# Kernel tuning notes

Measured on AMD Instinct MI355X. Metric: run time of the kernel, lower is better.

## Reference

```python
import jax, jax.numpy as jnp
import numpy as np

EPS = 1e-5


def _edge_conv(x, W, gamma, beta, k):
    """x: (B,N,C); W: (O,2C). Returns (B,N,O)."""
    xx = jnp.sum(x * x, axis=2, keepdims=True)                 # (B,N,1)
    inner = jnp.einsum('bnc,bmc->bnm', x, x)                   # (B,N,N)
    dist = xx + jnp.swapaxes(xx, 1, 2) - 2.0 * inner           # squared dists
    idx = jax.lax.top_k(-dist, k)[1]                           # (B,N,k) smallest dists
    nbr = jax.vmap(lambda xb, ib: xb[ib])(x, idx)              # (B,N,k,C) gather
    xi = jnp.broadcast_to(x[:, :, None, :], nbr.shape)
    edge = jnp.concatenate([nbr - xi, xi], axis=-1)            # (B,N,k,2C)
    out = jnp.einsum('bnkc,oc->bnko', edge, W)                 # 1x1 conv (per-edge linear)
    mean = jnp.mean(out, axis=(0, 1, 2))                       # BatchNorm2d (training stats)
    var = jnp.var(out, axis=(0, 1, 2))
    out = (out - mean) / jnp.sqrt(var + EPS) * gamma + beta
    return jnp.max(jax.nn.relu(out), axis=2)                   # max over k -> (B,N,O)


def _layernorm(x, g, b):
    mu = jnp.mean(x, axis=-1, keepdims=True)
    v = jnp.var(x, axis=-1, keepdims=True)
    return (x - mu) / jnp.sqrt(v + EPS) * g + b


def setup_inputs() -> dict:
    key = jax.random.key(0)
    ks = jax.random.split(key, 12)
    B, N = 8, 2048
    C1, C2, C3, C4 = 64, 64, 128, 256
    feat = C1 + C2 + C3 + C4              # 512
    fc_in = 2 * feat                      # max+avg -> 1024
    H, L = 512, 256

    def w(k_, shape):
        fan_in = shape[-1]
        return jax.random.normal(k_, shape, dtype=jnp.float32) * (1.0 / np.sqrt(fan_in))

    return {
        'points': jax.random.normal(ks[0], (B, N, 3), dtype=jnp.float32),
        'W1': w(ks[1], (C1, 6)),  'g1': jnp.ones(C1), 'b1': jnp.zeros(C1),
        'W2': w(ks[2], (C2, 2 * C1)), 'g2': jnp.ones(C2), 'b2': jnp.zeros(C2),
        'W3': w(ks[3], (C3, 2 * C2)), 'g3': jnp.ones(C3), 'b3': jnp.zeros(C3),
        'W4': w(ks[4], (C4, 2 * C3)), 'g4': jnp.ones(C4), 'b4': jnp.zeros(C4),
        'fc1_w': w(ks[5], (H, fc_in)), 'fc1_b': jnp.zeros(H),
        'ln1_g': jnp.ones(H), 'ln1_b': jnp.zeros(H),
        'fc2_w': w(ks[6], (L, H)), 'fc2_b': jnp.zeros(L),
        'ln2_g': jnp.ones(L), 'ln2_b': jnp.zeros(L),
        'k': 20,
    }


def reference(points, W1, g1, b1, W2, g2, b2, W3, g3, b3, W4, g4, b4,
              fc1_w, fc1_b, ln1_g, ln1_b, fc2_w, fc2_b, ln2_g, ln2_b, k):
    x1 = _edge_conv(points, W1, g1, b1, k)   # (B,N,64)
    x2 = _edge_conv(x1, W2, g2, b2, k)       # (B,N,64)
    x3 = _edge_conv(x2, W3, g3, b3, k)       # (B,N,128)
    x4 = _edge_conv(x3, W4, g4, b4, k)       # (B,N,256)
    feat = jnp.concatenate([x1, x2, x3, x4], axis=-1)          # (B,N,512)
    g = jnp.concatenate([jnp.max(feat, axis=1), jnp.mean(feat, axis=1)], axis=-1)  # (B,1024)
    h = g @ fc1_w.T + fc1_b
    h = jax.nn.relu(_layernorm(h, ln1_g, ln1_b))
    z = h @ fc2_w.T + fc2_b
    return _layernorm(z, ln2_g, ln2_b)       # (B,256)
```

## Files before the change

kernel.cpp:

```cpp
#include <hip/hip_runtime.h>
#include <cstdint>
#include <cstddef>

static constexpr int Bb = 8;
static constexpr int Nn = 2048;
static constexpr int Kn = 20;
static constexpr float EPSV = 1e-5f;


struct TransJobs {
    const float* in[6];
    float* out[6];
    int R[6];
    int Cc[6];
};

__global__ void transpose_all_kernel(TransJobs tj) {
    int m = blockIdx.y;
    int i = blockIdx.x * 256 + threadIdx.x;
    int total = tj.R[m] * tj.Cc[m];
    if (i < total) {
        int r = i / tj.Cc[m], c = i % tj.Cc[m];
        tj.out[m][(size_t)c * tj.R[m] + r] = tj.in[m][i];
    }
}


template<int C, int O>
__global__ void prep_kernel(const float* __restrict__ x, const float* __restrict__ wt,
                            float* __restrict__ z1, float* __restrict__ z2,
                            float* __restrict__ xx, float4* __restrict__ xp,
                            float* __restrict__ zp) {
    const int blk = blockIdx.x;
    const int tid = threadIdx.x;
    if (blk >= 1088) {
        zp[(blk - 1088) * 256 + tid] = 0.f;
        return;
    }
    if (blk >= 1024) {
        int i = (blk - 1024) * 256 + tid;
        const float* xr = x + (size_t)i * C;
        float s = 0.f;
        for (int c = 0; c < C; ++c) { float v = xr[c]; s += v * v; }
        xx[i] = s;
        if (C == 3) xp[i] = make_float4(xr[0], xr[1], xr[2], s);
        return;
    }
    constexpr int TP = 16;
    constexpr int G = 256 / O;
    constexpr int PP = TP / G;
    const int p0 = blk * TP;
    const int oo = tid % O;
    const int g = tid / O;
    __shared__ float xs[TP][(C < 4) ? 4 : C];
    for (int e = tid; e < TP * C; e += 256) {
        int p = e / C, c = e % C;
        xs[p][c] = x[(size_t)(p0 + p) * C + c];
    }
    __syncthreads();
    float a1[PP], a2[PP];
#pragma unroll
    for (int p = 0; p < PP; ++p) { a1[p] = 0.f; a2[p] = 0.f; }
    if constexpr (C % 4 == 0) {
        for (int c = 0; c < C; c += 4) {
            float w1[4], w2[4];
#pragma unroll
            for (int q = 0; q < 4; ++q) {
                w1[q] = wt[(size_t)(c + q) * O + oo];
                w2[q] = wt[(size_t)(C + c + q) * O + oo];
            }
#pragma unroll
            for (int p = 0; p < PP; ++p) {
                const float4 xv = *(const float4*)(&xs[g * PP + p][c]);
                a1[p] = fmaf(xv.w, w1[3], fmaf(xv.z, w1[2], fmaf(xv.y, w1[1], fmaf(xv.x, w1[0], a1[p]))));
                a2[p] = fmaf(xv.w, w2[3], fmaf(xv.z, w2[2], fmaf(xv.y, w2[1], fmaf(xv.x, w2[0], a2[p]))));
            }
        }
    } else {
        for (int c = 0; c < C; ++c) {
            float w1 = wt[(size_t)c * O + oo];
            float w2 = wt[(size_t)(C + c) * O + oo];
#pragma unroll
            for (int p = 0; p < PP; ++p) {
                float xv = xs[g * PP + p][c];
                a1[p] = fmaf(xv, w1, a1[p]);
                a2[p] = fmaf(xv, w2, a2[p]);
            }
        }
    }
#pragma unroll
    for (int p = 0; p < PP; ++p) {
        size_t row = (size_t)(p0 + g * PP + p) * O + oo;
        z1[row] = a1[p];
        z2[row] = a2[p];
    }
}


using half8 = __attribute__((ext_vector_type(8))) _Float16;
using f32x16 = __attribute__((ext_vector_type(16))) float;

template<int C>
__global__ __launch_bounds__(256, 2)
void gram_dist_kernel(const float* __restrict__ x, const float* __restrict__ xx,
                      float* __restrict__ dist, int b0, size_t dstride) {
    static_assert(C % 32 == 0, "CT=32 tiling");
    constexpr int CT = 32;
    const int b = b0 + blockIdx.z;
    int p = blockIdx.x, rblk = 0;
    while (p >= 16 - rblk) { p -= 16 - rblk; ++rblk; }
    const int cblk = rblk + p;
    const int i0 = rblk * 128, j0 = cblk * 128;
    const int tid = threadIdx.x;
    const int lane = tid & 63;
    const int wv = tid >> 6;
    const int wr = wv >> 1, wc = wv & 1;

    __shared__ __align__(16) unsigned char smem[32768];
    _Float16* const AH = (_Float16*)smem;
    _Float16* const AL = AH + 4096;
    _Float16* const BH = AH + 8192;
    _Float16* const BL = AH + 12288;
    float (*T)[132] = (float (*)[132])smem;

    const float* xb = x + (size_t)b * Nn * C;
    int sga[4];
    const float* sgs[4];
#pragma unroll
    for (int q = 0; q < 4; ++q) {
        int g = tid + 256 * q;
        int pnt = (g >> 2) & 127;
        int cb8 = g & 3;
        sga[q] = cb8 * 128 + (pnt & ~7) + ((pnt + 2 * cb8) & 7);
        sgs[q] = xb + (size_t)(((q < 2) ? i0 : j0) + pnt) * C + cb8 * 8;
    }

    int fa[2][2], fb[2][2];
#pragma unroll
    for (int ks = 0; ks < 2; ++ks)
#pragma unroll
        for (int mi = 0; mi < 2; ++mi) {
            int t8 = ks * 2 + (lane >> 5);
            int pa = wr * 64 + mi * 32 + (lane & 31);
            int pb = wc * 64 + mi * 32 + (lane & 31);
            fa[ks][mi] = t8 * 128 + (pa & ~7) + ((pa + 2 * t8) & 7);
            fb[ks][mi] = t8 * 128 + (pb & ~7) + ((pb + 2 * t8) & 7);
        }

    f32x16 ahh[2][2] = {};
    f32x16 axx[2][2] = {};

    for (int c0 = 0; c0 < C; c0 += CT) {
#pragma unroll
        for (int q = 0; q < 4; ++q) {
            const float4 f0 = *(const float4*)(sgs[q] + c0);
            const float4 f1 = *(const float4*)(sgs[q] + c0 + 4);
            float v[8] = {f0.x, f0.y, f0.z, f0.w, f1.x, f1.y, f1.z, f1.w};
            half8 hv, lv;
#pragma unroll
            for (int e = 0; e < 8; ++e) {
                _Float16 h = (_Float16)v[e];
                hv[e] = h;
                lv[e] = (_Float16)((v[e] - (float)h) * 4096.f);
            }
            _Float16* dh = (q < 2) ? AH : BH;
            _Float16* dl = (q < 2) ? AL : BL;
            *(half8*)(dh + sga[q] * 8) = hv;
            *(half8*)(dl + sga[q] * 8) = lv;
        }
        __syncthreads();
#pragma unroll
        for (int ks = 0; ks < 2; ++ks) {
            half8 ah[2], al[2], bh[2], bl[2];
#pragma unroll
            for (int mi = 0; mi < 2; ++mi) {
                ah[mi] = *(const half8*)(AH + fa[ks][mi] * 8);
                al[mi] = *(const half8*)(AL + fa[ks][mi] * 8);
                bh[mi] = *(const half8*)(BH + fb[ks][mi] * 8);
                bl[mi] = *(const half8*)(BL + fb[ks][mi] * 8);
            }
#pragma unroll
            for (int mi = 0; mi < 2; ++mi)
#pragma unroll
                for (int ni = 0; ni < 2; ++ni) {
                    ahh[mi][ni] = __builtin_amdgcn_mfma_f32_32x32x16_f16(ah[mi], bh[ni], ahh[mi][ni], 0, 0, 0);
                    axx[mi][ni] = __builtin_amdgcn_mfma_f32_32x32x16_f16(ah[mi], bl[ni], axx[mi][ni], 0, 0, 0);
                    axx[mi][ni] = __builtin_amdgcn_mfma_f32_32x32x16_f16(al[mi], bh[ni], axx[mi][ni], 0, 0, 0);
                }
        }
        __syncthreads();
    }

    const float* xxb = xx + (size_t)b * Nn;
    float xi[2][16];
#pragma unroll
    for (int mi = 0; mi < 2; ++mi)
#pragma unroll
        for (int g = 0; g < 4; ++g) {
            float4 t4 = *(const float4*)(xxb + i0 + wr * 64 + mi * 32 + 4 * (lane >> 5) + 8 * g);
            xi[mi][g * 4 + 0] = t4.x; xi[mi][g * 4 + 1] = t4.y;
            xi[mi][g * 4 + 2] = t4.z; xi[mi][g * 4 + 3] = t4.w;
        }
    float xj[2];
#pragma unroll
    for (int ni = 0; ni < 2; ++ni) xj[ni] = xxb[j0 + wc * 64 + ni * 32 + (lane & 31)];

    float* db = dist + (size_t)blockIdx.z * dstride;
#pragma unroll
    for (int mi = 0; mi < 2; ++mi)
#pragma unroll
        for (int ni = 0; ni < 2; ++ni) {
            const int col = j0 + wc * 64 + ni * 32 + (lane & 31);
#pragma unroll
            for (int r = 0; r < 16; ++r) {
                int row = i0 + wr * 64 + mi * 32 + (r & 3) + 8 * (r >> 2) + 4 * (lane >> 5);
                float inner = fmaf(axx[mi][ni][r], 2.44140625e-4f, ahh[mi][ni][r]);
                db[(size_t)row * Nn + col] = xi[mi][r] + xj[ni] - 2.f * inner;
            }
        }

    if (cblk > rblk) {
        const int rr = tid >> 3;
        const int c4 = (tid & 7) * 4;
#pragma unroll
        for (int m = 0; m < 4; ++m) {
            if (wc == (m >> 1)) {
#pragma unroll
                for (int mi = 0; mi < 2; ++mi)
#pragma unroll
                    for (int r = 0; r < 16; ++r) {
                        int ig = wr * 64 + mi * 32 + (r & 3) + 8 * (r >> 2) + 4 * (lane >> 5);
                        if ((m & 1) == 0) {
                            float inner = fmaf(axx[mi][0][r], 2.44140625e-4f, ahh[mi][0][r]);
                            T[lane & 31][ig] = xi[mi][r] + xj[0] - 2.f * inner;
                        } else {
                            float inner = fmaf(axx[mi][1][r], 2.44140625e-4f, ahh[mi][1][r]);
                            T[lane & 31][ig] = xi[mi][r] + xj[1] - 2.f * inner;
                        }
                    }
            }
            __syncthreads();
            float* orow = db + (size_t)(j0 + m * 32 + rr) * Nn + i0;
#pragma unroll
            for (int s = 0; s < 4; ++s)
                *(float4*)(orow + c4 + s * 32) = *(const float4*)&T[rr][c4 + s * 32];
            __syncthreads();
        }
    }
}


template<int CTRL>
__device__ __forceinline__ float dpp_min_step(float v) {
    int x = __float_as_int(v);
    int y = __builtin_amdgcn_update_dpp(x, x, CTRL, 0xf, 0xf, false);
    return fminf(v, __int_as_float(y));
}

__device__ __forceinline__ float wave_min64(float v) {
    v = dpp_min_step<0x111>(v);
    v = dpp_min_step<0x112>(v);
    v = dpp_min_step<0x114>(v);
    v = dpp_min_step<0x118>(v);
    v = dpp_min_step<0x142>(v);
    v = dpp_min_step<0x143>(v);
    return __int_as_float(__builtin_amdgcn_readlane(__float_as_int(v), 63));
}

__device__ __forceinline__ float pack_key(float v, int m) {
    return __int_as_float((__float_as_int(v) & ~31) | m);
}

#define TOP4_INS(v)                                                               \
    {                                                                             \
        bool l3 = (v) < tv3;                                                      \
        if (l3) {                                                                 \
            bool l2 = (v) < tv2;                                                  \
            bool l1 = (v) < tv1;                                                  \
            bool l0 = (v) < tv0;                                                  \
            tv3 = l2 ? tv2 : (v);                                                 \
            tv2 = l2 ? (l1 ? tv1 : (v)) : tv2;                                    \
            tv1 = l1 ? (l0 ? tv0 : (v)) : tv1;                                    \
            tv0 = l0 ? (v) : tv0;                                                 \
        }                                                                         \
    }

__device__ __forceinline__ void top4_build(const float4* __restrict__ dr4, int lane,
                                           float lvk,
                                           float& tv0, float& tv1, float& tv2, float& tv3) {
    tv0 = tv1 = tv2 = tv3 = 3e38f;
#pragma unroll
    for (int q = 0; q < 8; ++q) {
        float4 f = dr4[q * 64 + lane];
        float vv[4] = {f.x, f.y, f.z, f.w};
#pragma unroll
        for (int c = 0; c < 4; ++c) {
            float vk = pack_key(vv[c], q * 4 + c);
            if (vk > lvk) TOP4_INS(vk)
        }
    }
}

#define TOPK_ROUNDS(REBUILD, DECODE)                                              \
    int myj = 0;                                                                  \
    for (int t = 0; t < Kn; ++t) {                                                \
        float bv = wave_min64(tv0);                                               \
        unsigned long long tied = __ballot(tv0 == bv);                            \
        int wl = (int)(__ffsll((long long)tied) - 1);                             \
        int bm = __float_as_int(bv) & 31;                                         \
        int bj = (DECODE);                                                        \
        if (lane == t) myj = bj;                                                  \
        if (tv0 == bv && lane == wl) {                                            \
            tv0 = tv1; tv1 = tv2; tv2 = tv3; tv3 = 3e38f;                         \
            if (tv0 == 3e38f) { REBUILD; }                                        \
        }                                                                         \
    }                                                                             \
    if (lane < Kn) orow[lane] = myj;

__global__ void topk_kernel(const float* __restrict__ dist, int* __restrict__ idxo,
                            int b0, size_t dstride, int rows_per_batch_only) {
    const int w = threadIdx.x >> 6;
    const int lane = threadIdx.x & 63;
    const int lin = blockIdx.x * 4 + w;
    int bz, i;
    if (rows_per_batch_only) { bz = 0; i = lin; }
    else { bz = lin >> 11; i = lin & (Nn - 1); }
    const int b = b0 + bz;
    const float4* dr4 = (const float4*)(dist + (size_t)bz * dstride + (size_t)i * Nn);

    float tv0, tv1, tv2, tv3;
    top4_build(dr4, lane, -3e38f, tv0, tv1, tv2, tv3);

    int* orow = idxo + ((size_t)b * Nn + i) * Kn;
    TOPK_ROUNDS(top4_build(dr4, lane, bv, tv0, tv1, tv2, tv3),
                (bm >> 2) * 256 + wl * 4 + (bm & 3))
}


__device__ __forceinline__ void top4_build_c3(const float4* __restrict__ xpb,
                                              float xi0, float xi1, float xi2, float xxi,
                                              int lane, float lvk,
                                              float& tv0, float& tv1, float& tv2, float& tv3) {
    tv0 = tv1 = tv2 = tv3 = 3e38f;
#pragma unroll
    for (int m = 0; m < 32; ++m) {
        float4 f = xpb[m * 64 + lane];
        float acc = 0.f;
        acc = fmaf(xi0, f.x, acc);
        acc = fmaf(xi1, f.y, acc);
        acc = fmaf(xi2, f.z, acc);
        float v = xxi + f.w - 2.f * acc;
        float vk = pack_key(v, m);
        if (vk > lvk) TOP4_INS(vk)
    }
}

__global__ void topk_c3_kernel(const float4* __restrict__ xp, int* __restrict__ idxo,
                               int b0, int rows_per_batch_only) {
    const int w = threadIdx.x >> 6;
    const int lane = threadIdx.x & 63;
    const int lin = blockIdx.x * 4 + w;
    int bz, i;
    if (rows_per_batch_only) { bz = 0; i = lin; }
    else { bz = lin >> 11; i = lin & (Nn - 1); }
    const int b = b0 + bz;
    const float4* xpb = xp + (size_t)b * Nn;
    const float4 fi = xpb[i];
    const float xi0 = fi.x, xi1 = fi.y, xi2 = fi.z, xxi = fi.w;

    float tv0, tv1, tv2, tv3;
    top4_build_c3(xpb, xi0, xi1, xi2, xxi, lane, -3e38f, tv0, tv1, tv2, tv3);

    int* orow = idxo + ((size_t)b * Nn + i) * Kn;
    TOPK_ROUNDS(top4_build_c3(xpb, xi0, xi1, xi2, xxi, lane, bv, tv0, tv1, tv2, tv3),
                bm * 64 + wl)
}


template<int O>
__global__ void edge_stats_kernel(const float* __restrict__ z1, const float* __restrict__ z2,
                                  const int* __restrict__ idx,
                                  float* __restrict__ vmax, float* __restrict__ vmin,
                                  float* __restrict__ ssum, float* __restrict__ ssq) {
    constexpr int TPP = O / 4;
    constexpr int PPB = 256 / TPP;
    const int p0 = blockIdx.x * PPB;
    const int tid = threadIdx.x;
    const int q = tid % TPP;
    const int p = tid / TPP;
    const int oo = q * 4;
    __shared__ int jl[PPB][Kn];
    for (int e = tid; e < PPB * Kn; e += 256)
        jl[e / Kn][e % Kn] = idx[(size_t)(p0 + e / Kn) * Kn + (e % Kn)];
    __syncthreads();
    const int bi = p0 + p;
    const int b = bi >> 11;
    const float4 zi1 = *(const float4*)(z1 + (size_t)bi * O + oo);
    const float4 zi2 = *(const float4*)(z2 + (size_t)bi * O + oo);
    float ax = zi2.x - zi1.x, ay = zi2.y - zi1.y, az = zi2.z - zi1.z, aw = zi2.w - zi1.w;
    float mxx = -3e38f, mxy = -3e38f, mxz = -3e38f, mxw = -3e38f;
    float mnx = 3e38f, mny = 3e38f, mnz = 3e38f, mnw = 3e38f;
    float sx = 0.f, sy = 0.f, sz = 0.f, sw = 0.f;
    float qx = 0.f, qy = 0.f, qz = 0.f, qw = 0.f;
    const float* zbase = z1 + ((size_t)b * Nn) * O + oo;
#pragma unroll
    for (int kk = 0; kk < Kn; ++kk) {
        int j = jl[p][kk];
        float4 v = *(const float4*)(zbase + (size_t)j * O);
        v.x += ax; v.y += ay; v.z += az; v.w += aw;
        mxx = fmaxf(mxx, v.x); mxy = fmaxf(mxy, v.y); mxz = fmaxf(mxz, v.z); mxw = fmaxf(mxw, v.w);
        mnx = fminf(mnx, v.x); mny = fminf(mny, v.y); mnz = fminf(mnz, v.z); mnw = fminf(mnw, v.w);
        sx += v.x; sy += v.y; sz += v.z; sw += v.w;
        qx = fmaf(v.x, v.x, qx); qy = fmaf(v.y, v.y, qy);
        qz = fmaf(v.z, v.z, qz); qw = fmaf(v.w, v.w, qw);
    }
    float4 mx4 = make_float4(mxx, mxy, mxz, mxw);
    float4 mn4 = make_float4(mnx, mny, mnz, mnw);
    *(float4*)(vmax + (size_t)bi * O + oo) = mx4;
    *(float4*)(vmin + (size_t)bi * O + oo) = mn4;
    __shared__ float4 ssm[256], sqq[256];
    ssm[tid] = make_float4(sx, sy, sz, sw);
    sqq[tid] = make_float4(qx, qy, qz, qw);
    __syncthreads();
    if (p == 0) {
#pragma unroll 4
        for (int pp = 1; pp < PPB; ++pp) {
            float4 s4 = ssm[pp * TPP + q];
            float4 q4 = sqq[pp * TPP + q];
            sx += s4.x; sy += s4.y; sz += s4.z; sw += s4.w;
            qx += q4.x; qy += q4.y; qz += q4.z; qw += q4.w;
        }
        int slot = blockIdx.x & 63;
        atomicAdd(&ssum[slot * O + oo + 0], sx);
        atomicAdd(&ssum[slot * O + oo + 1], sy);
        atomicAdd(&ssum[slot * O + oo + 2], sz);
        atomicAdd(&ssum[slot * O + oo + 3], sw);
        atomicAdd(&ssq[slot * O + oo + 0], qx);
        atomicAdd(&ssq[slot * O + oo + 1], qy);
        atomicAdd(&ssq[slot * O + oo + 2], qz);
        atomicAdd(&ssq[slot * O + oo + 3], qw);
    }
}


template<int O>
__global__ void apply_pool_kernel(const float* __restrict__ vmax, const float* __restrict__ vmin,
                                  const float* __restrict__ ssum, const float* __restrict__ ssq,
                                  const float* __restrict__ gamma, const float* __restrict__ beta,
                                  float* __restrict__ xout,
                                  float* __restrict__ pmax, float* __restrict__ psum, int obase) {
    constexpr int TPP = O / 4;
    constexpr int PP2 = 256 / TPP;
    constexpr int S = 128 / PP2;
    const int chunk = blockIdx.x;
    const int b = blockIdx.y;
    const int tid = threadIdx.x;
    const int q = tid % TPP;
    const int g = tid / TPP;
    const int oo = q * 4;
    __shared__ __align__(16) float lsc[O], lsh[O];
    for (int o = tid; o < O; o += 256) {
        float s = 0.f, qq = 0.f;
        for (int sl = 0; sl < 64; ++sl) { s += ssum[sl * O + o]; qq += ssq[sl * O + o]; }
        const float cnt = (float)Bb * (float)Nn * (float)Kn;
        float mu = s / cnt;
        float var = qq / cnt - mu * mu;
        float sc_ = gamma[o] / sqrtf(var + EPSV);
        lsc[o] = sc_;
        lsh[o] = beta[o] - mu * sc_;
    }
    __syncthreads();
    const float4 sc = *(const float4*)(lsc + oo);
    const float4 sh = *(const float4*)(lsh + oo);
    float pmx = -3e38f, pmy = -3e38f, pmz = -3e38f, pmw = -3e38f;
    float psx = 0.f, psy = 0.f, psz = 0.f, psw = 0.f;
    const int n0 = chunk * 128;
    for (int s = 0; s < S; ++s) {
        int n = n0 + g + s * PP2;
        size_t ix = ((size_t)b * Nn + n) * O + oo;
        float4 vx = *(const float4*)(vmax + ix);
        float4 vn = *(const float4*)(vmin + ix);
        float4 r;
        r.x = fmaxf(fmaf(sc.x >= 0.f ? vx.x : vn.x, sc.x, sh.x), 0.f);
        r.y = fmaxf(fmaf(sc.y >= 0.f ? vx.y : vn.y, sc.y, sh.y), 0.f);
        r.z = fmaxf(fmaf(sc.z >= 0.f ? vx.z : vn.z, sc.z, sh.z), 0.f);
        r.w = fmaxf(fmaf(sc.w >= 0.f ? vx.w : vn.w, sc.w, sh.w), 0.f);
        *(float4*)(xout + ix) = r;
        pmx = fmaxf(pmx, r.x); pmy = fmaxf(pmy, r.y);
        pmz = fmaxf(pmz, r.z); pmw = fmaxf(pmw, r.w);
        psx += r.x; psy += r.y; psz += r.z; psw += r.w;
    }
    __shared__ float4 sm[256], ss2[256];
    sm[tid] = make_float4(pmx, pmy, pmz, pmw);
    ss2[tid] = make_float4(psx, psy, psz, psw);
    __syncthreads();
    if (g == 0) {
#pragma unroll 4
        for (int gg = 1; gg < PP2; ++gg) {
            float4 m4 = sm[gg * TPP + q];
            float4 s4 = ss2[gg * TPP + q];
            pmx = fmaxf(pmx, m4.x); pmy = fmaxf(pmy, m4.y);
            pmz = fmaxf(pmz, m4.z); pmw = fmaxf(pmw, m4.w);
            psx += s4.x; psy += s4.y; psz += s4.z; psw += s4.w;
        }
        size_t pb = ((size_t)b * 16 + chunk) * 512 + obase + oo;
        *(float4*)(pmax + pb) = make_float4(pmx, pmy, pmz, pmw);
        *(float4*)(psum + pb) = make_float4(psx, psy, psz, psw);
    }
}


__global__ void head1_kernel(const float* __restrict__ pmax, const float* __restrict__ psum,
                             const float* __restrict__ fct1, float* __restrict__ hp1) {
    const int ks = blockIdx.x;
    const int b = blockIdx.y;
    const int tid = threadIdx.x;
    __shared__ float gxs[64];
    if (tid < 64) {
        int c = ks * 64 + tid;
        if (c < 512) {
            float mx = -3e38f;
            for (int ch = 0; ch < 16; ++ch)
                mx = fmaxf(mx, pmax[((size_t)b * 16 + ch) * 512 + c]);
            gxs[tid] = mx;
        } else {
            int e = c - 512;
            float s = 0.f;
            for (int ch = 0; ch < 16; ++ch)
                s += psum[((size_t)b * 16 + ch) * 512 + e];
            gxs[tid] = s * (1.f / (float)Nn);
        }
    }
    __syncthreads();
    float h0 = 0.f, h1 = 0.f;
    const float* w = fct1 + (size_t)(ks * 64) * 512;
    for (int c = 0; c < 64; ++c) {
        float gc = gxs[c];
        h0 = fmaf(gc, w[(size_t)c * 512 + tid], h0);
        h1 = fmaf(gc, w[(size_t)c * 512 + tid + 256], h1);
    }
    hp1[((size_t)b * 16 + ks) * 512 + tid] = h0;
    hp1[((size_t)b * 16 + ks) * 512 + tid + 256] = h1;
}

__global__ void head2_kernel(const float* __restrict__ hp1, const float* __restrict__ fc1b,
                             const float* __restrict__ ln1g, const float* __restrict__ ln1b,
                             float* __restrict__ hh) {
    const int b = blockIdx.x;
    const int tid = threadIdx.x;
    __shared__ float red[256];
    float h0 = fc1b[tid], h1 = fc1b[tid + 256];
    for (int ks = 0; ks < 16; ++ks) {
        h0 += hp1[((size_t)b * 16 + ks) * 512 + tid];
        h1 += hp1[((size_t)b * 16 + ks) * 512 + tid + 256];
    }
    red[tid] = h0 + h1;
    __syncthreads();
    for (int st = 128; st > 0; st >>= 1) { if (tid < st) red[tid] += red[tid + st]; __syncthreads(); }
    float mu = red[0] * (1.f / 512.f);
    __syncthreads();
    float d0 = h0 - mu, d1 = h1 - mu;
    red[tid] = d0 * d0 + d1 * d1;
    __syncthreads();
    for (int st = 128; st > 0; st >>= 1) { if (tid < st) red[tid] += red[tid + st]; __syncthreads(); }
    float rs = 1.f / sqrtf(red[0] * (1.f / 512.f) + EPSV);
    hh[(size_t)b * 512 + tid]       = fmaxf(d0 * rs * ln1g[tid] + ln1b[tid], 0.f);
    hh[(size_t)b * 512 + tid + 256] = fmaxf(d1 * rs * ln1g[tid + 256] + ln1b[tid + 256], 0.f);
}

__global__ void head3_kernel(const float* __restrict__ hh, const float* __restrict__ fct2,
                             float* __restrict__ hp2) {
    const int ks = blockIdx.x;
    const int b = blockIdx.y;
    const int tid = threadIdx.x;
    __shared__ float hs[128];
    if (tid < 128) hs[tid] = hh[(size_t)b * 512 + ks * 128 + tid];
    __syncthreads();
    float z = 0.f;
    const float* w = fct2 + (size_t)(ks * 128) * 256;
    for (int c = 0; c < 128; ++c)
        z = fmaf(hs[c], w[(size_t)c * 256 + tid], z);
    hp2[((size_t)b * 4 + ks) * 256 + tid] = z;
}

__global__ void head4_kernel(const float* __restrict__ hp2, const float* __restrict__ fc2b,
                             const float* __restrict__ ln2g, const float* __restrict__ ln2b,
                             float* __restrict__ out) {
    const int b = blockIdx.x;
    const int tid = threadIdx.x;
    __shared__ float red[256];
    float z = fc2b[tid];
    for (int ks = 0; ks < 4; ++ks) z += hp2[((size_t)b * 4 + ks) * 256 + tid];
    red[tid] = z;
    __syncthreads();
    for (int st = 128; st > 0; st >>= 1) { if (tid < st) red[tid] += red[tid + st]; __syncthreads(); }
    float mu2 = red[0] * (1.f / 256.f);
    __syncthreads();
    float dz = z - mu2;
    red[tid] = dz * dz;
    __syncthreads();
    for (int st = 128; st > 0; st >>= 1) { if (tid < st) red[tid] += red[tid + st]; __syncthreads(); }
    float rs2 = 1.f / sqrtf(red[0] * (1.f / 256.f) + EPSV);
    out[b * 256 + tid] = dz * rs2 * ln2g[tid] + ln2b[tid];
}


template<int C, int O>
static void run_layer(const float* x, const float* gamma, const float* beta,
                      float* xout, float* DIST, float* XX, float4* XP, int* IDX,
                      float* Z1, float* Z2,
                      float* VMX, float* VMN, float* SSUM, float* SSQ,
                      const float* WT, float* PMAX, float* PSUM, int obase, bool big,
                      hipStream_t stream) {
    prep_kernel<C, O><<<1216, 256, 0, stream>>>(x, WT, Z1, Z2, XX, XP, SSUM);
    if constexpr (C == 3) {
        if (big) {
            topk_c3_kernel<<<Bb * Nn / 4, 256, 0, stream>>>(XP, IDX, 0, 0);
        } else {
            for (int b = 0; b < Bb; ++b)
                topk_c3_kernel<<<Nn / 4, 256, 0, stream>>>(XP, IDX, b, 1);
        }
    } else {
        if (big) {
            gram_dist_kernel<C><<<dim3(136, 1, Bb), 256, 0, stream>>>(x, XX, DIST, 0, (size_t)Nn * Nn);
            topk_kernel<<<Bb * Nn / 4, 256, 0, stream>>>(DIST, IDX, 0, (size_t)Nn * Nn, 0);
        } else {
            for (int b = 0; b < Bb; ++b) {
                gram_dist_kernel<C><<<dim3(136, 1, 1), 256, 0, stream>>>(x, XX, DIST, b, 0);
                topk_kernel<<<Nn / 4, 256, 0, stream>>>(DIST, IDX, b, 0, 1);
            }
        }
    }
    edge_stats_kernel<O><<<Bb * Nn / (1024 / O), 256, 0, stream>>>(Z1, Z2, IDX, VMX, VMN, SSUM, SSQ);
    apply_pool_kernel<O><<<dim3(16, 8), 256, 0, stream>>>(VMX, VMN, SSUM, SSQ, gamma, beta,
                                                          xout, PMAX, PSUM, obase);
}

extern "C" void kernel_launch(void* const* d_in, const int* in_sizes, int n_in,
                              void* d_out, int out_size, void* d_ws, size_t ws_size,
                              hipStream_t stream) {
    const float* points = (const float*)d_in[0];
    const float* W1 = (const float*)d_in[1];
    const float* g1 = (const float*)d_in[2];
    const float* b1 = (const float*)d_in[3];
    const float* W2 = (const float*)d_in[4];
    const float* g2 = (const float*)d_in[5];
    const float* b2 = (const float*)d_in[6];
    const float* W3 = (const float*)d_in[7];
    const float* g3 = (const float*)d_in[8];
    const float* b3 = (const float*)d_in[9];
    const float* W4 = (const float*)d_in[10];
    const float* g4 = (const float*)d_in[11];
    const float* b4 = (const float*)d_in[12];
    const float* fc1_w = (const float*)d_in[13];
    const float* fc1_b = (const float*)d_in[14];
    const float* ln1g = (const float*)d_in[15];
    const float* ln1b = (const float*)d_in[16];
    const float* fc2_w = (const float*)d_in[17];
    const float* fc2_b = (const float*)d_in[18];
    const float* ln2g = (const float*)d_in[19];
    const float* ln2b = (const float*)d_in[20];

    float* ws = (float*)d_ws;
    const size_t BN = (size_t)Bb * Nn;
    const bool big = ws_size >= (size_t)59826688 * 4;

    size_t off = 0;
    auto take = [&](size_t n) { size_t o = off; off += n; return o; };
    float* DIST = ws + take(big ? (size_t)Bb * Nn * Nn : (size_t)Nn * Nn);
    float* XX   = ws + take(BN);
    float4* XP  = (float4*)(ws + take(BN * 4));
    int*   IDX  = (int*)(ws + take(BN * Kn));
    float* Z1   = ws + take(BN * 256);
    float* Z2   = ws + take(BN * 256);
    float* VMX  = ws + take(BN * 256);
    float* VMN  = ws + take(BN * 256);
    float* SSUM = ws + take(64 * 256);
    float* SSQ  = ws + take(64 * 256);
    float* WT1  = ws + take(384);
    float* WT2  = ws + take(8192);
    float* WT3  = ws + take(16384);
    float* WT4  = ws + take(65536);
    float* FCT1 = ws + take(524288);
    float* FCT2 = ws + take(131072);
    float* X1   = ws + take(BN * 64);
    float* X2   = ws + take(BN * 64);
    float* X3   = ws + take(BN * 128);
    float* X4   = ws + take(BN * 256);
    float* PMAX = ws + take((size_t)Bb * 16 * 512);
    float* PSUM = ws + take((size_t)Bb * 16 * 512);

    float* HP1 = DIST;
    float* HH  = DIST + 65536;
    float* HP2 = DIST + 65536 + 4096;

    TransJobs tj;
    tj.in[0] = W1;    tj.out[0] = WT1;  tj.R[0] = 64;  tj.Cc[0] = 6;
    tj.in[1] = W2;    tj.out[1] = WT2;  tj.R[1] = 64;  tj.Cc[1] = 128;
    tj.in[2] = W3;    tj.out[2] = WT3;  tj.R[2] = 128; tj.Cc[2] = 128;
    tj.in[3] = W4;    tj.out[3] = WT4;  tj.R[3] = 256; tj.Cc[3] = 256;
    tj.in[4] = fc1_w; tj.out[4] = FCT1; tj.R[4] = 512; tj.Cc[4] = 1024;
    tj.in[5] = fc2_w; tj.out[5] = FCT2; tj.R[5] = 256; tj.Cc[5] = 512;
    transpose_all_kernel<<<dim3(2048, 6), 256, 0, stream>>>(tj);

    run_layer<3, 64>(points, g1, b1, X1, DIST, XX, XP, IDX, Z1, Z2, VMX, VMN, SSUM, SSQ, WT1, PMAX, PSUM, 0, big, stream);
    run_layer<64, 64>(X1, g2, b2, X2, DIST, XX, XP, IDX, Z1, Z2, VMX, VMN, SSUM, SSQ, WT2, PMAX, PSUM, 64, big, stream);
    run_layer<64, 128>(X2, g3, b3, X3, DIST, XX, XP, IDX, Z1, Z2, VMX, VMN, SSUM, SSQ, WT3, PMAX, PSUM, 128, big, stream);
    run_layer<128, 256>(X3, g4, b4, X4, DIST, XX, XP, IDX, Z1, Z2, VMX, VMN, SSUM, SSQ, WT4, PMAX, PSUM, 256, big, stream);

    head1_kernel<<<dim3(16, 8), 256, 0, stream>>>(PMAX, PSUM, FCT1, HP1);
    head2_kernel<<<Bb, 256, 0, stream>>>(HP1, fc1_b, ln1g, ln1b, HH);
    head3_kernel<<<dim3(4, 8), 256, 0, stream>>>(HH, FCT2, HP2);
    head4_kernel<<<Bb, 256, 0, stream>>>(HP2, fc2_b, ln2g, ln2b, (float*)d_out);
}
```

Baseline: 542.1 us.

## Compute per-point edge projections with split-fp16 MFMA instead of scalar FMA

For layers 2-4, the per-point projections Z1/Z2 (x times the two halves of W) are now computed with 32x32x16 fp16 MFMA instructions. Each fp32 input is split into a high fp16 part and a scaled low residual, and three MFMA products keep close to fp32 accuracy. A new prep kernel does the split into the DIST scratch buffer and also computes the squared norms and zeroes the stats. This replaces the scalar FMA GEMM and the weight transposes for those layers, at the cost of an extra kernel launch, extra memory traffic for the split buffers, and a small accuracy risk.

```diff
diff --git a/kernel.cpp b/kernel.cpp
--- a/kernel.cpp
+++ b/kernel.cpp
@@ -24,6 +24,9 @@
         tj.out[m][(size_t)c * tj.R[m] + r] = tj.in[m][i];
     }
 }
+
+using half8 = __attribute__((ext_vector_type(8))) _Float16;
+using f32x16 = __attribute__((ext_vector_type(16))) float;
 
 
 template<int C, int O>
@@ -61,31 +64,14 @@
     float a1[PP], a2[PP];
 #pragma unroll
     for (int p = 0; p < PP; ++p) { a1[p] = 0.f; a2[p] = 0.f; }
-    if constexpr (C % 4 == 0) {
-        for (int c = 0; c < C; c += 4) {
-            float w1[4], w2[4];
-#pragma unroll
-            for (int q = 0; q < 4; ++q) {
-                w1[q] = wt[(size_t)(c + q) * O + oo];
-                w2[q] = wt[(size_t)(C + c + q) * O + oo];
-            }
-#pragma unroll
-            for (int p = 0; p < PP; ++p) {
-                const float4 xv = *(const float4*)(&xs[g * PP + p][c]);
-                a1[p] = fmaf(xv.w, w1[3], fmaf(xv.z, w1[2], fmaf(xv.y, w1[1], fmaf(xv.x, w1[0], a1[p]))));
-                a2[p] = fmaf(xv.w, w2[3], fmaf(xv.z, w2[2], fmaf(xv.y, w2[1], fmaf(xv.x, w2[0], a2[p]))));
-            }
-        }
-    } else {
-        for (int c = 0; c < C; ++c) {
-            float w1 = wt[(size_t)c * O + oo];
-            float w2 = wt[(size_t)(C + c) * O + oo];
-#pragma unroll
-            for (int p = 0; p < PP; ++p) {
-                float xv = xs[g * PP + p][c];
-                a1[p] = fmaf(xv, w1, a1[p]);
-                a2[p] = fmaf(xv, w2, a2[p]);
-            }
+    for (int c = 0; c < C; ++c) {
+        float w1 = wt[(size_t)c * O + oo];
+        float w2 = wt[(size_t)(C + c) * O + oo];
+#pragma unroll
+        for (int p = 0; p < PP; ++p) {
+            float xv = xs[g * PP + p][c];
+            a1[p] = fmaf(xv, w1, a1[p]);
+            a2[p] = fmaf(xv, w2, a2[p]);
         }
     }
 #pragma unroll
@@ -97,8 +83,90 @@
 }
 
 
-using half8 = __attribute__((ext_vector_type(8))) _Float16;
-using f32x16 = __attribute__((ext_vector_type(16))) float;
+template<int C, int O>
+__global__ void slim_prep_kernel(const float* __restrict__ x, const float* __restrict__ w,
+                                 _Float16* __restrict__ xh, _Float16* __restrict__ xl,
+                                 _Float16* __restrict__ wh, _Float16* __restrict__ wl,
+                                 float* __restrict__ xx, float* __restrict__ zp) {
+    constexpr int NXS = (Bb * Nn * C) / 2048;
+    constexpr int NWS = (O * 2 * C) / 2048;
+    static_assert((Bb * Nn * C) % 2048 == 0 && (O * 2 * C) % 2048 == 0, "split tiling");
+    const int blk = blockIdx.x;
+    const int tid = threadIdx.x;
+    if (blk < NXS + NWS) {
+        const bool isw = blk >= NXS;
+        const float* src = isw ? w : x;
+        _Float16* dh = isw ? wh : xh;
+        _Float16* dl = isw ? wl : xl;
+        size_t idx = ((size_t)(isw ? blk - NXS : blk) * 256 + tid) * 8;
+        float4 f0 = *(const float4*)(src + idx);
+        float4 f1 = *(const float4*)(src + idx + 4);
+        float v[8] = {f0.x, f0.y, f0.z, f0.w, f1.x, f1.y, f1.z, f1.w};
+        half8 hv, lv;
+#pragma unroll
+        for (int e = 0; e < 8; ++e) {
+            _Float16 h = (_Float16)v[e];
+            hv[e] = h;
+            lv[e] = (_Float16)((v[e] - (float)h) * 4096.f);
+        }
+        *(half8*)(dh + idx) = hv;
+        *(half8*)(dl + idx) = lv;
+        return;
+    }
+    int b2 = blk - NXS - NWS;
+    if (b2 < 64) {
+        int i = b2 * 256 + tid;
+        const float* xr = x + (size_t)i * C;
+        float s = 0.f;
+        for (int c = 0; c < C; ++c) { float v = xr[c]; s += v * v; }
+        xx[i] = s;
+        return;
+    }
+    zp[(b2 - 64) * 256 + tid] = 0.f;
+}
+
+
+template<int C, int O>
+__global__ __launch_bounds__(256)
+void zmfma_kernel(const _Float16* __restrict__ xh, const _Float16* __restrict__ xl,
+                  const _Float16* __restrict__ wh, const _Float16* __restrict__ wl,
+                  float* __restrict__ z1, float* __restrict__ z2) {
+    static_assert(C % 16 == 0 && O % 32 == 0, "tiling");
+    const int tid = threadIdx.x;
+    const int lane = tid & 63;
+    const int wv = tid >> 6;
+    const int wr = wv >> 1, wc = wv & 1;
+    const int p = blockIdx.x * 64 + wr * 32 + (lane & 31);
+    const int gcol = blockIdx.y * 64 + wc * 32 + (lane & 31);
+    const int s = (gcol >= O) ? 1 : 0;
+    const int o = gcol - s * O;
+    const int k8 = (lane >> 5) * 8;
+    const _Float16* ap_h = xh + (size_t)p * C + k8;
+    const _Float16* ap_l = xl + (size_t)p * C + k8;
+    const _Float16* bp_h = wh + (size_t)o * (2 * C) + s * C + k8;
+    const _Float16* bp_l = wl + (size_t)o * (2 * C) + s * C + k8;
+
+    f32x16 hh = {};
+    f32x16 xs = {};
+#pragma unroll
+    for (int k = 0; k < C; k += 16) {
+        half8 ah = *(const half8*)(ap_h + k);
+        half8 al = *(const half8*)(ap_l + k);
+        half8 bh = *(const half8*)(bp_h + k);
+        half8 bl = *(const half8*)(bp_l + k);
+        hh = __builtin_amdgcn_mfma_f32_32x32x16_f16(ah, bh, hh, 0, 0, 0);
+        xs = __builtin_amdgcn_mfma_f32_32x32x16_f16(ah, bl, xs, 0, 0, 0);
+        xs = __builtin_amdgcn_mfma_f32_32x32x16_f16(al, bh, xs, 0, 0, 0);
+    }
+    float* out = s ? z2 : z1;
+    const int rbase = blockIdx.x * 64 + wr * 32 + 4 * (lane >> 5);
+#pragma unroll
+    for (int r = 0; r < 16; ++r) {
+        int row = rbase + (r & 3) + 8 * (r >> 2);
+        out[(size_t)row * O + o] = fmaf(xs[r], 2.44140625e-4f, hh[r]);
+    }
+}
+
 
 template<int C>
 __global__ __launch_bounds__(256, 2)
@@ -606,14 +674,14 @@
 
 
 template<int C, int O>
-static void run_layer(const float* x, const float* gamma, const float* beta,
+static void run_layer(const float* x, const float* W, const float* gamma, const float* beta,
                       float* xout, float* DIST, float* XX, float4* XP, int* IDX,
                       float* Z1, float* Z2,
                       float* VMX, float* VMN, float* SSUM, float* SSQ,
                       const float* WT, float* PMAX, float* PSUM, int obase, bool big,
                       hipStream_t stream) {
-    prep_kernel<C, O><<<1216, 256, 0, stream>>>(x, WT, Z1, Z2, XX, XP, SSUM);
     if constexpr (C == 3) {
+        prep_kernel<C, O><<<1216, 256, 0, stream>>>(x, WT, Z1, Z2, XX, XP, SSUM);
         if (big) {
             topk_c3_kernel<<<Bb * Nn / 4, 256, 0, stream>>>(XP, IDX, 0, 0);
         } else {
@@ -621,6 +689,16 @@
                 topk_c3_kernel<<<Nn / 4, 256, 0, stream>>>(XP, IDX, b, 1);
         }
     } else {
+        _Float16* XH = (_Float16*)DIST;
+        _Float16* XL = XH + (size_t)Bb * Nn * C;
+        _Float16* WH = XL + (size_t)Bb * Nn * C;
+        _Float16* WL = WH + (size_t)O * 2 * C;
+        constexpr int NXS = (Bb * Nn * C) / 2048;
+        constexpr int NWS = (O * 2 * C) / 2048;
+        slim_prep_kernel<C, O><<<NXS + NWS + 64 + 128, 256, 0, stream>>>(
+            x, W, XH, XL, WH, WL, XX, SSUM);
+        zmfma_kernel<C, O><<<dim3(Bb * Nn / 64, 2 * O / 64), 256, 0, stream>>>(
+            XH, XL, WH, WL, Z1, Z2);
         if (big) {
             gram_dist_kernel<C><<<dim3(136, 1, Bb), 256, 0, stream>>>(x, XX, DIST, 0, (size_t)Nn * Nn);
             topk_kernel<<<Bb * Nn / 4, 256, 0, stream>>>(DIST, IDX, 0, (size_t)Nn * Nn, 0);
@@ -689,6 +767,7 @@
     float* X4   = ws + take(BN * 256);
     float* PMAX = ws + take((size_t)Bb * 16 * 512);
     float* PSUM = ws + take((size_t)Bb * 16 * 512);
+    (void)WT2; (void)WT3; (void)WT4;
 
     float* HP1 = DIST;
     float* HH  = DIST + 65536;
@@ -696,17 +775,14 @@
 
     TransJobs tj;
     tj.in[0] = W1;    tj.out[0] = WT1;  tj.R[0] = 64;  tj.Cc[0] = 6;
-    tj.in[1] = W2;    tj.out[1] = WT2;  tj.R[1] = 64;  tj.Cc[1] = 128;
-    tj.in[2] = W3;    tj.out[2] = WT3;  tj.R[2] = 128; tj.Cc[2] = 128;
-    tj.in[3] = W4;    tj.out[3] = WT4;  tj.R[3] = 256; tj.Cc[3] = 256;
-    tj.in[4] = fc1_w; tj.out[4] = FCT1; tj.R[4] = 512; tj.Cc[4] = 1024;
-    tj.in[5] = fc2_w; tj.out[5] = FCT2; tj.R[5] = 256; tj.Cc[5] = 512;
-    transpose_all_kernel<<<dim3(2048, 6), 256, 0, stream>>>(tj);
-
-    run_layer<3, 64>(points, g1, b1, X1, DIST, XX, XP, IDX, Z1, Z2, VMX, VMN, SSUM, SSQ, WT1, PMAX, PSUM, 0, big, stream);
-    run_layer<64, 64>(X1, g2, b2, X2, DIST, XX, XP, IDX, Z1, Z2, VMX, VMN, SSUM, SSQ, WT2, PMAX, PSUM, 64, big, stream);
-    run_layer<64, 128>(X2, g3, b3, X3, DIST, XX, XP, IDX, Z1, Z2, VMX, VMN, SSUM, SSQ, WT3, PMAX, PSUM, 128, big, stream);
-    run_layer<128, 256>(X3, g4, b4, X4, DIST, XX, XP, IDX, Z1, Z2, VMX, VMN, SSUM, SSQ, WT4, PMAX, PSUM, 256, big, stream);
+    tj.in[1] = fc1_w; tj.out[1] = FCT1; tj.R[1] = 512; tj.Cc[1] = 1024;
+    tj.in[2] = fc2_w; tj.out[2] = FCT2; tj.R[2] = 256; tj.Cc[2] = 512;
+    transpose_all_kernel<<<dim3(2048, 3), 256, 0, stream>>>(tj);
+
+    run_layer<3, 64>(points, W1, g1, b1, X1, DIST, XX, XP, IDX, Z1, Z2, VMX, VMN, SSUM, SSQ, WT1, PMAX, PSUM, 0, big, stream);
+    run_layer<64, 64>(X1, W2, g2, b2, X2, DIST, XX, XP, IDX, Z1, Z2, VMX, VMN, SSUM, SSQ, WT1, PMAX, PSUM, 64, big, stream);
+    run_layer<64, 128>(X2, W3, g3, b3, X3, DIST, XX, XP, IDX, Z1, Z2, VMX, VMN, SSUM, SSQ, WT1, PMAX, PSUM, 128, big, stream);
+    run_layer<128, 256>(X3, W4, g4, b4, X4, DIST, XX, XP, IDX, Z1, Z2, VMX, VMN, SSUM, SSQ, WT1, PMAX, PSUM, 256, big, stream);
 
     head1_kernel<<<dim3(16, 8), 256, 0, stream>>>(PMAX, PSUM, FCT1, HP1);
     head2_kernel<<<Bb, 256, 0, stream>>>(HP1, fc1_b, ln1g, ln1b, HH);
```

New measurement: 539.4 us. About the same (-0.5%).

## Compute per-point edge-conv projections with split-fp16 MFMA GEMM

Applied to the files above, without the earlier changes.

For layers 2-4, the per-point linear projections Z1/Z2 now come from a new MFMA kernel instead of scalar FMAs in prep_kernel. That kernel reads W directly with no transpose and uses hi/lo fp16 splitting to keep near-fp32 accuracy. A slim prep kernel now only computes squared norms and zeroes the stats buffers, and the weight transposes for W2-W4 are dropped. The aim is to cut the FMA-bound projection cost, at the price of three MFMAs per tile and small precision differences from the fp16 split.

```diff
diff --git a/kernel.cpp b/kernel.cpp
--- a/kernel.cpp
+++ b/kernel.cpp
@@ -24,6 +24,9 @@
         tj.out[m][(size_t)c * tj.R[m] + r] = tj.in[m][i];
     }
 }
+
+using half8 = __attribute__((ext_vector_type(8))) _Float16;
+using f32x16 = __attribute__((ext_vector_type(16))) float;
 
 
 template<int C, int O>
@@ -61,31 +64,14 @@
     float a1[PP], a2[PP];
 #pragma unroll
     for (int p = 0; p < PP; ++p) { a1[p] = 0.f; a2[p] = 0.f; }
-    if constexpr (C % 4 == 0) {
-        for (int c = 0; c < C; c += 4) {
-            float w1[4], w2[4];
-#pragma unroll
-            for (int q = 0; q < 4; ++q) {
-                w1[q] = wt[(size_t)(c + q) * O + oo];
-                w2[q] = wt[(size_t)(C + c + q) * O + oo];
-            }
-#pragma unroll
-            for (int p = 0; p < PP; ++p) {
-                const float4 xv = *(const float4*)(&xs[g * PP + p][c]);
-                a1[p] = fmaf(xv.w, w1[3], fmaf(xv.z, w1[2], fmaf(xv.y, w1[1], fmaf(xv.x, w1[0], a1[p]))));
-                a2[p] = fmaf(xv.w, w2[3], fmaf(xv.z, w2[2], fmaf(xv.y, w2[1], fmaf(xv.x, w2[0], a2[p]))));
-            }
-        }
-    } else {
-        for (int c = 0; c < C; ++c) {
-            float w1 = wt[(size_t)c * O + oo];
-            float w2 = wt[(size_t)(C + c) * O + oo];
-#pragma unroll
-            for (int p = 0; p < PP; ++p) {
-                float xv = xs[g * PP + p][c];
-                a1[p] = fmaf(xv, w1, a1[p]);
-                a2[p] = fmaf(xv, w2, a2[p]);
-            }
+    for (int c = 0; c < C; ++c) {
+        float w1 = wt[(size_t)c * O + oo];
+        float w2 = wt[(size_t)(C + c) * O + oo];
+#pragma unroll
+        for (int p = 0; p < PP; ++p) {
+            float xv = xs[g * PP + p][c];
+            a1[p] = fmaf(xv, w1, a1[p]);
+            a2[p] = fmaf(xv, w2, a2[p]);
         }
     }
 #pragma unroll
@@ -97,8 +83,132 @@
 }
 
 
-using half8 = __attribute__((ext_vector_type(8))) _Float16;
-using f32x16 = __attribute__((ext_vector_type(16))) float;
+template<int C>
+__global__ void slim2_prep_kernel(const float* __restrict__ x,
+                                  float* __restrict__ xx, float* __restrict__ zp) {
+    const int blk = blockIdx.x;
+    const int tid = threadIdx.x;
+    if (blk < 64) {
+        int i = blk * 256 + tid;
+        const float* xr = x + (size_t)i * C;
+        float s = 0.f;
+        for (int c = 0; c < C; ++c) { float v = xr[c]; s += v * v; }
+        xx[i] = s;
+        return;
+    }
+    zp[(blk - 64) * 256 + tid] = 0.f;
+}
+
+
+template<int C, int O>
+__global__ __launch_bounds__(256, 2)
+void zmfma_kernel(const float* __restrict__ x, const float* __restrict__ w,
+                  float* __restrict__ z1, float* __restrict__ z2) {
+    static_assert(C % 32 == 0 && (2 * O) % 128 == 0 && O >= 64, "tiling");
+    constexpr int CT = 32;
+    const int i0 = blockIdx.x * 128;
+    const int j0 = blockIdx.y * 128;
+    const int tid = threadIdx.x;
+    const int lane = tid & 63;
+    const int wv = tid >> 6;
+    const int wr = wv >> 1, wc = wv & 1;
+
+    __shared__ __align__(16) unsigned char smem[32768];
+    _Float16* const AH = (_Float16*)smem;
+    _Float16* const AL = AH + 4096;
+    _Float16* const BH = AH + 8192;
+    _Float16* const BL = AH + 12288;
+
+    int sga[4];
+    const float* sgs[4];
+#pragma unroll
+    for (int q = 0; q < 4; ++q) {
+        int g = tid + 256 * q;
+        int pnt = (g >> 2) & 127;
+        int cb8 = g & 3;
+        sga[q] = cb8 * 128 + (pnt & ~7) + ((pnt + 2 * cb8) & 7);
+        if (q < 2) {
+            sgs[q] = x + (size_t)(i0 + pnt) * C + cb8 * 8;
+        } else {
+            int gcol = j0 + pnt;
+            int s = (gcol >= O) ? 1 : 0;
+            int o = gcol - s * O;
+            sgs[q] = w + (size_t)o * (2 * C) + s * C + cb8 * 8;
+        }
+    }
+
+    int fa[2][2], fb[2][2];
+#pragma unroll
+    for (int ks = 0; ks < 2; ++ks)
+#pragma unroll
+        for (int mi = 0; mi < 2; ++mi) {
+            int t8 = ks * 2 + (lane >> 5);
+            int pa = wr * 64 + mi * 32 + (lane & 31);
+            int pb = wc * 64 + mi * 32 + (lane & 31);
+            fa[ks][mi] = t8 * 128 + (pa & ~7) + ((pa + 2 * t8) & 7);
+            fb[ks][mi] = t8 * 128 + (pb & ~7) + ((pb + 2 * t8) & 7);
+        }
+
+    f32x16 ahh[2][2] = {};
+    f32x16 axx[2][2] = {};
+
+    for (int c0 = 0; c0 < C; c0 += CT) {
+#pragma unroll
+        for (int q = 0; q < 4; ++q) {
+            const float4 f0 = *(const float4*)(sgs[q] + c0);
+            const float4 f1 = *(const float4*)(sgs[q] + c0 + 4);
+            float v[8] = {f0.x, f0.y, f0.z, f0.w, f1.x, f1.y, f1.z, f1.w};
+            half8 hv, lv;
+#pragma unroll
+            for (int e = 0; e < 8; ++e) {
+                _Float16 h = (_Float16)v[e];
+                hv[e] = h;
+                lv[e] = (_Float16)((v[e] - (float)h) * 4096.f);
+            }
+            _Float16* dh = (q < 2) ? AH : BH;
+            _Float16* dl = (q < 2) ? AL : BL;
+            *(half8*)(dh + sga[q] * 8) = hv;
+            *(half8*)(dl + sga[q] * 8) = lv;
+        }
+        __syncthreads();
+#pragma unroll
+        for (int ks = 0; ks < 2; ++ks) {
+            half8 ah[2], al[2], bh[2], bl[2];
+#pragma unroll
+            for (int mi = 0; mi < 2; ++mi) {
+                ah[mi] = *(const half8*)(AH + fa[ks][mi] * 8);
+                al[mi] = *(const half8*)(AL + fa[ks][mi] * 8);
+                bh[mi] = *(const half8*)(BH + fb[ks][mi] * 8);
+                bl[mi] = *(const half8*)(BL + fb[ks][mi] * 8);
+            }
+#pragma unroll
+            for (int mi = 0; mi < 2; ++mi)
+#pragma unroll
+                for (int ni = 0; ni < 2; ++ni) {
+                    ahh[mi][ni] = __builtin_amdgcn_mfma_f32_32x32x16_f16(ah[mi], bh[ni], ahh[mi][ni], 0, 0, 0);
+                    axx[mi][ni] = __builtin_amdgcn_mfma_f32_32x32x16_f16(ah[mi], bl[ni], axx[mi][ni], 0, 0, 0);
+                    axx[mi][ni] = __builtin_amdgcn_mfma_f32_32x32x16_f16(al[mi], bh[ni], axx[mi][ni], 0, 0, 0);
+                }
+        }
+        __syncthreads();
+    }
+
+#pragma unroll
+    for (int mi = 0; mi < 2; ++mi)
+#pragma unroll
+        for (int ni = 0; ni < 2; ++ni) {
+            const int cb = wc * 64 + ni * 32;
+            const int s = ((j0 + cb) >= O) ? 1 : 0;
+            float* outp = s ? z2 : z1;
+            const int o = j0 + cb - s * O + (lane & 31);
+#pragma unroll
+            for (int r = 0; r < 16; ++r) {
+                int row = i0 + wr * 64 + mi * 32 + (r & 3) + 8 * (r >> 2) + 4 * (lane >> 5);
+                outp[(size_t)row * O + o] = fmaf(axx[mi][ni][r], 2.44140625e-4f, ahh[mi][ni][r]);
+            }
+        }
+}
+
 
 template<int C>
 __global__ __launch_bounds__(256, 2)
@@ -606,14 +716,14 @@
 
 
 template<int C, int O>
-static void run_layer(const float* x, const float* gamma, const float* beta,
+static void run_layer(const float* x, const float* W, const float* gamma, const float* beta,
                       float* xout, float* DIST, float* XX, float4* XP, int* IDX,
                       float* Z1, float* Z2,
                       float* VMX, float* VMN, float* SSUM, float* SSQ,
                       const float* WT, float* PMAX, float* PSUM, int obase, bool big,
                       hipStream_t stream) {
-    prep_kernel<C, O><<<1216, 256, 0, stream>>>(x, WT, Z1, Z2, XX, XP, SSUM);
     if constexpr (C == 3) {
+        prep_kernel<C, O><<<1216, 256, 0, stream>>>(x, WT, Z1, Z2, XX, XP, SSUM);
         if (big) {
             topk_c3_kernel<<<Bb * Nn / 4, 256, 0, stream>>>(XP, IDX, 0, 0);
         } else {
@@ -621,6 +731,8 @@
                 topk_c3_kernel<<<Nn / 4, 256, 0, stream>>>(XP, IDX, b, 1);
         }
     } else {
+        slim2_prep_kernel<C><<<192, 256, 0, stream>>>(x, XX, SSUM);
+        zmfma_kernel<C, O><<<dim3(Bb * Nn / 128, 2 * O / 128), 256, 0, stream>>>(x, W, Z1, Z2);
         if (big) {
             gram_dist_kernel<C><<<dim3(136, 1, Bb), 256, 0, stream>>>(x, XX, DIST, 0, (size_t)Nn * Nn);
             topk_kernel<<<Bb * Nn / 4, 256, 0, stream>>>(DIST, IDX, 0, (size_t)Nn * Nn, 0);
@@ -689,6 +801,7 @@
     float* X4   = ws + take(BN * 256);
     float* PMAX = ws + take((size_t)Bb * 16 * 512);
     float* PSUM = ws + take((size_t)Bb * 16 * 512);
+    (void)WT2; (void)WT3; (void)WT4;
 
     float* HP1 = DIST;
     float* HH  = DIST + 65536;
@@ -696,17 +809,14 @@
 
     TransJobs tj;
     tj.in[0] = W1;    tj.out[0] = WT1;  tj.R[0] = 64;  tj.Cc[0] = 6;
-    tj.in[1] = W2;    tj.out[1] = WT2;  tj.R[1] = 64;  tj.Cc[1] = 128;
-    tj.in[2] = W3;    tj.out[2] = WT3;  tj.R[2] = 128; tj.Cc[2] = 128;
-    tj.in[3] = W4;    tj.out[3] = WT4;  tj.R[3] = 256; tj.Cc[3] = 256;
-    tj.in[4] = fc1_w; tj.out[4] = FCT1; tj.R[4] = 512; tj.Cc[4] = 1024;
-    tj.in[5] = fc2_w; tj.out[5] = FCT2; tj.R[5] = 256; tj.Cc[5] = 512;
-    transpose_all_kernel<<<dim3(2048, 6), 256, 0, stream>>>(tj);
-
-    run_layer<3, 64>(points, g1, b1, X1, DIST, XX, XP, IDX, Z1, Z2, VMX, VMN, SSUM, SSQ, WT1, PMAX, PSUM, 0, big, stream);
-    run_layer<64, 64>(X1, g2, b2, X2, DIST, XX, XP, IDX, Z1, Z2, VMX, VMN, SSUM, SSQ, WT2, PMAX, PSUM, 64, big, stream);
-    run_layer<64, 128>(X2, g3, b3, X3, DIST, XX, XP, IDX, Z1, Z2, VMX, VMN, SSUM, SSQ, WT3, PMAX, PSUM, 128, big, stream);
-    run_layer<128, 256>(X3, g4, b4, X4, DIST, XX, XP, IDX, Z1, Z2, VMX, VMN, SSUM, SSQ, WT4, PMAX, PSUM, 256, big, stream);
+    tj.in[1] = fc1_w; tj.out[1] = FCT1; tj.R[1] = 512; tj.Cc[1] = 1024;
+    tj.in[2] = fc2_w; tj.out[2] = FCT2; tj.R[2] = 256; tj.Cc[2] = 512;
+    transpose_all_kernel<<<dim3(2048, 3), 256, 0, stream>>>(tj);
+
+    run_layer<3, 64>(points, W1, g1, b1, X1, DIST, XX, XP, IDX, Z1, Z2, VMX, VMN, SSUM, SSQ, WT1, PMAX, PSUM, 0, big, stream);
+    run_layer<64, 64>(X1, W2, g2, b2, X2, DIST, XX, XP, IDX, Z1, Z2, VMX, VMN, SSUM, SSQ, WT1, PMAX, PSUM, 64, big, stream);
+    run_layer<64, 128>(X2, W3, g3, b3, X3, DIST, XX, XP, IDX, Z1, Z2, VMX, VMN, SSUM, SSQ, WT1, PMAX, PSUM, 128, big, stream);
+    run_layer<128, 256>(X3, W4, g4, b4, X4, DIST, XX, XP, IDX, Z1, Z2, VMX, VMN, SSUM, SSQ, WT1, PMAX, PSUM, 256, big, stream);
 
     head1_kernel<<<dim3(16, 8), 256, 0, stream>>>(PMAX, PSUM, FCT1, HP1);
     head2_kernel<<<Bb, 256, 0, stream>>>(HP1, fc1_b, ln1g, ln1b, HH);
```

Result: slower. 559.1 us (+3.1%).
